# Kernel tuning notes

Hardware: AMD Instinct MI355X
Metric: run time of the kernel (lower is better)

The kernel has to match this reference:

```python
import jax, jax.numpy as jnp
import numpy as np

N_NODES = 200000
N_EDGES = 1250000
N_RELS = 8
IN_F, HID_F, OUT_F = 64, 64, 32


def setup_inputs() -> dict:
    key = jax.random.key(0)
    ks = jax.random.split(key, 8)
    x = jax.random.normal(ks[0], (N_NODES, IN_F), dtype=jnp.float32)
    edge_index = jax.random.randint(ks[1], (2, N_EDGES), 0, N_NODES, dtype=jnp.int64)
    edge_type = jax.random.randint(ks[2], (N_EDGES,), 0, N_RELS, dtype=jnp.int64)
    # Glorot-ish scaled params
    weight1 = jax.random.normal(ks[3], (N_RELS, IN_F, HID_F), dtype=jnp.float32) / np.sqrt(IN_F)
    root1 = jax.random.normal(ks[4], (IN_F, HID_F), dtype=jnp.float32) / np.sqrt(IN_F)
    bias1 = jnp.zeros((HID_F,), dtype=jnp.float32)
    weight2 = jax.random.normal(ks[5], (N_RELS, HID_F, OUT_F), dtype=jnp.float32) / np.sqrt(HID_F)
    root2 = jax.random.normal(ks[6], (HID_F, OUT_F), dtype=jnp.float32) / np.sqrt(HID_F)
    bias2 = jnp.zeros((OUT_F,), dtype=jnp.float32)
    return {"x": x, "edge_index": edge_index, "edge_type": edge_type,
            "weight1": weight1, "root1": root1, "bias1": bias1,
            "weight2": weight2, "root2": root2, "bias2": bias2}


def _rgcn_conv(x, edge_src, edge_dst, edge_type, weight, root, bias):
    """PyG RGCNConv: per-relation mean aggregation + root transform + bias."""
    num_nodes = x.shape[0]
    num_rels = weight.shape[0]
    # Transform every node under every relation weight: [N, R, H]
    xw = jnp.einsum('nd,rdh->nrh', x, weight)
    # Per-edge message: source node transformed by the edge's relation weight
    msgs = xw[edge_src, edge_type]  # [E, H]
    # Per-(target node, relation) mean aggregation
    seg = edge_dst * num_rels + edge_type  # combined segment id
    num_seg = num_nodes * num_rels
    sums = jax.ops.segment_sum(msgs, seg, num_segments=num_seg)  # [N*R, H]
    cnts = jax.ops.segment_sum(jnp.ones((msgs.shape[0],), dtype=x.dtype), seg,
                               num_segments=num_seg)
    mean = sums / jnp.maximum(cnts, 1.0)[:, None]
    agg = mean.reshape(num_nodes, num_rels, -1).sum(axis=1)  # sum over relations
    return agg + x @ root + bias


def reference(x, edge_index, edge_type, weight1, root1, bias1, weight2, root2, bias2):
    edge_src, edge_dst = edge_index[0], edge_index[1]
    h = _rgcn_conv(x, edge_src, edge_dst, edge_type, weight1, root1, bias1)
    h = jax.nn.relu(h)
    out = _rgcn_conv(h, edge_src, edge_dst, edge_type, weight2, root2, bias2)
    return out
```

## Files before the change

### kernel.cpp

```cpp
#include <hip/hip_runtime.h>

#define N_NODES 200000
#define N_EDGES 1250000
#define N_RELS 8
#define NROWS 1600000
#define NROWS_PAD 1601536
#define NSCAN 782
#define NBUCK 6250

#define NB_COUNT 4883
#define NB_XCAST 6250
#define NB_PREP1 144
#define NB_PREP2 72

typedef __attribute__((ext_vector_type(8))) short short8v;
typedef __attribute__((ext_vector_type(4))) float f32x4;

__device__ __forceinline__ ushort rne_bf16(float v) {
  unsigned u = __float_as_uint(v);
  return (ushort)((u + 0x7FFFu + ((u >> 16) & 1u)) >> 16);
}


__device__ __forceinline__ void prep_body(const float* W, const float* Root,
                                          ushort* Bf, int ncol, int i) {
  int col = i / 576, k = i - col * 576;
  float w = (k < 512) ? W[k * ncol + col] : Root[(k - 512) * ncol + col];
  int WN = ncol >> 4;
  int ks = k >> 5, kg = (k >> 3) & 3, j = k & 7;
  int wn = col >> 4, l15 = col & 15;
  int lane = (kg << 4) | l15;
  Bf[(ks * WN + wn) * 512 + lane * 8 + j] = rne_bf16(w);
}

__global__ __launch_bounds__(256) void k_setup(
    const int* __restrict__ ei, const int* __restrict__ et, int* __restrict__ cnt,
    const float* __restrict__ x, ushort* __restrict__ xbf,
    const float* __restrict__ w1, const float* __restrict__ r1, ushort* __restrict__ bf1,
    const float* __restrict__ w2, const float* __restrict__ r2, ushort* __restrict__ bf2) {
  int blk = blockIdx.x, t = threadIdx.x;
  if (blk < NB_COUNT) {
    int e = blk * 256 + t;
    if (e < N_EDGES) {
      int dst = ei[N_EDGES + e];
      int r = et[e];
      atomicAdd(&cnt[dst * N_RELS + r], 1);
    }
  } else if (blk < NB_COUNT + NB_XCAST) {
    int i = (blk - NB_COUNT) * 256 + t;
    float4 a = ((const float4*)x)[i * 2];
    float4 b = ((const float4*)x)[i * 2 + 1];
    union { uint4 q; ushort u[8]; } o;
    o.u[0] = rne_bf16(a.x); o.u[1] = rne_bf16(a.y);
    o.u[2] = rne_bf16(a.z); o.u[3] = rne_bf16(a.w);
    o.u[4] = rne_bf16(b.x); o.u[5] = rne_bf16(b.y);
    o.u[6] = rne_bf16(b.z); o.u[7] = rne_bf16(b.w);
    ((uint4*)xbf)[i] = o.q;
  } else if (blk < NB_COUNT + NB_XCAST + NB_PREP1) {
    int i = (blk - NB_COUNT - NB_XCAST) * 256 + t;
    prep_body(w1, r1, bf1, 64, i);
  } else {
    int i = (blk - NB_COUNT - NB_XCAST - NB_PREP1) * 256 + t;
    prep_body(w2, r2, bf2, 32, i);
  }
}


__global__ __launch_bounds__(256) void k_bsum(const int* __restrict__ cnt,
                                              int* __restrict__ bsum) {
  __shared__ int sh[256];
  int b = blockIdx.x, t = threadIdx.x;
  const int4* p = (const int4*)(cnt + b * 2048);
  int4 v0 = p[2 * t], v1 = p[2 * t + 1];
  int s = v0.x + v0.y + v0.z + v0.w + v1.x + v1.y + v1.z + v1.w;
  sh[t] = s;
  __syncthreads();
  for (int o = 128; o >= 1; o >>= 1) {
    if (t < o) sh[t] += sh[t + o];
    __syncthreads();
  }
  if (t == 0) bsum[b] = sh[0];
}

__global__ __launch_bounds__(1024) void k_scan1(const int* __restrict__ bsum,
                                                int* __restrict__ bpre,
                                                int* __restrict__ rowoff) {
  __shared__ int sh[1024];
  int t = threadIdx.x;
  int v = (t < NSCAN) ? bsum[t] : 0;
  sh[t] = v;
  __syncthreads();
  for (int o = 1; o < 1024; o <<= 1) {
    int a = (t >= o) ? sh[t - o] : 0;
    __syncthreads();
    sh[t] += a;
    __syncthreads();
  }
  if (t < NSCAN) bpre[t] = sh[t] - v;
  if (t == 0) rowoff[NROWS] = N_EDGES;
}

__global__ __launch_bounds__(256) void k_apply(const int* __restrict__ cnt,
                                               const int* __restrict__ bpre,
                                               int* __restrict__ rowoff,
                                               int* __restrict__ cursor) {
  __shared__ int sh[256];
  int b = blockIdx.x, t = threadIdx.x;
  const int4* p = (const int4*)(cnt + b * 2048);
  int4 v0 = p[2 * t], v1 = p[2 * t + 1];
  int v[8] = {v0.x, v0.y, v0.z, v0.w, v1.x, v1.y, v1.z, v1.w};
  int s = 0;
#pragma unroll
  for (int j = 0; j < 8; ++j) s += v[j];
  sh[t] = s;
  __syncthreads();
  for (int o = 1; o < 256; o <<= 1) {
    int a = (t >= o) ? sh[t - o] : 0;
    __syncthreads();
    sh[t] += a;
    __syncthreads();
  }
  int run = bpre[b] + sh[t] - s;
  int base = b * 2048 + t * 8;
#pragma unroll
  for (int j = 0; j < 8; ++j) {
    int i = base + j;
    if (i < NROWS) { rowoff[i] = run; cursor[i] = run; }
    run += v[j];
  }
}

__global__ void k_scatter(const int* __restrict__ ei, const int* __restrict__ et,
                          int* __restrict__ cursor, int* __restrict__ ep) {
  int e = blockIdx.x * 256 + threadIdx.x;
  if (e < N_EDGES) {
    int src = ei[e];
    int dst = ei[N_EDGES + e];
    int r = et[e];
    int row = dst * N_RELS + r;
    int pos = atomicAdd(&cursor[row], 1);
    ep[pos] = src | ((row & 255) << 18);
  }
}


template <int NCOL, bool RELUOUT, bool OUTBF>
__global__ __launch_bounds__(512, 8) void k_rgcn(
    const ushort* __restrict__ Xg, const ushort* __restrict__ Bf,
    const float* __restrict__ Bias, const int* __restrict__ rowoff,
    const int* __restrict__ ep, void* __restrict__ OutP) {
  __shared__ __align__(16) ushort agg[256 * 64];
  __shared__ int loff[260];
  __shared__ int wsplit[12];
  __shared__ __align__(16) float bias_lds[64];

  int t = threadIdx.x;
  int b = blockIdx.x;
  int d0 = b * 32;
  int lane = t & 63, w = t >> 6;

  {
    uint4 zz = make_uint4(0, 0, 0, 0);
    uint4* a4 = (uint4*)agg;
#pragma unroll
    for (int q = 0; q < 4; ++q) a4[t + q * 512] = zz;
  }
  if (t < 257) loff[t] = rowoff[b * 256 + t];
  if (t < NCOL) bias_lds[t] = Bias[t];
  __syncthreads();
  if (t < 9) {
    int s0 = loff[0], ntot = loff[256] - s0;
    int target = s0 + ((ntot * t) >> 3);
    int lo = 0, hi = 256;
    while (lo < hi) {
      int mid = (lo + hi) >> 1;
      if (loff[mid] < target) lo = mid + 1; else hi = mid;
    }
    wsplit[t] = lo;
  }
  __syncthreads();

  {
    int s = __builtin_amdgcn_readfirstlane(loff[wsplit[w]]);
    int e = __builtin_amdgcn_readfirstlane(loff[wsplit[w + 1]]);
    int n = e - s;
    const int* wep = ep + s;
    const char* Xb = (const char*)Xg;
    unsigned lane2 = (unsigned)(lane << 1);
    int cur = -1, nrun = 0;
    float a = 0.f;

#define FLUSH()                                                         \
    {                                                                   \
      float m = a * __builtin_amdgcn_rcpf((float)nrun);                 \
      int sw = (cur << 6) + (lane ^ (((cur >> 3) & 7) << 3));           \
      agg[sw] = rne_bf16(m);                                            \
    }

    int i = 0;
    for (; i + 8 <= n; i += 8) {
      int pk[8];
#pragma unroll
      for (int u = 0; u < 8; ++u)
        pk[u] = __builtin_amdgcn_readfirstlane(wep[i + u]);
      ushort hv[8];
#pragma unroll
      for (int u = 0; u < 8; ++u)
        hv[u] = *(const ushort*)(Xb + ((((unsigned)pk[u] & 0x3FFFFu) << 7) + lane2));
#pragma unroll
      for (int u = 0; u < 8; ++u) {
        int row = (int)((unsigned)pk[u] >> 18);
        float v = __uint_as_float((unsigned)hv[u] << 16);
        if (row != cur) {
          if (cur >= 0) FLUSH();
          cur = row; a = 0.f; nrun = 0;
        }
        a += v; ++nrun;
      }
    }
    for (; i < n; ++i) {
      int pk = __builtin_amdgcn_readfirstlane(wep[i]);
      ushort hv = *(const ushort*)(Xb + ((((unsigned)pk & 0x3FFFFu) << 7) + lane2));
      int row = (int)((unsigned)pk >> 18);
      float v = __uint_as_float((unsigned)hv << 16);
      if (row != cur) {
        if (cur >= 0) FLUSH();
        cur = row; a = 0.f; nrun = 0;
      }
      a += v; ++nrun;
    }
    if (cur >= 0) FLUSH();
#undef FLUSH
  }
  __syncthreads();

  int l15 = lane & 15, kg = lane >> 4;
  f32x4 acc = {0.f, 0.f, 0.f, 0.f};

  if constexpr (NCOL == 64) {
    int wm = w >> 2, wn = w & 3;
    int col = wn * 16 + l15;
    for (int ks = 0; ks < 18; ++ks) {
      union { uint4 q; short8v s; } bh, ah;
      bh.q = *(const uint4*)(Bf + (ks * 4 + wn) * 512 + lane * 8);
      if (ks < 16) {
        int rr = ks >> 1;
        int f0 = ((ks & 1) << 5) + (kg << 3);
        int row = ((wm * 16 + l15) << 3) + rr;
        int sw = (row << 6) + (f0 ^ ((l15 & 7) << 3));
        ah.q = *(const uint4*)&agg[sw];
      } else {
        int kb = ((ks - 16) << 5) + (kg << 3);
        ah.q = *(const uint4*)&Xg[(size_t)(d0 + wm * 16 + l15) * 64 + kb];
      }
      acc = __builtin_amdgcn_mfma_f32_16x16x32_bf16(ah.s, bh.s, acc, 0, 0, 0);
    }
#pragma unroll
    for (int i2 = 0; i2 < 4; ++i2) {
      float v = acc[i2] + bias_lds[col];
      if (RELUOUT) v = fmaxf(v, 0.f);
      size_t o = (size_t)(d0 + wm * 16 + kg * 4 + i2) * 64 + col;
      if (OUTBF) ((ushort*)OutP)[o] = rne_bf16(v);
      else ((float*)OutP)[o] = v;
    }
  } else {
    int wm = w >> 2, wn = (w >> 1) & 1, ksp = w & 1;
    int col = wn * 16 + l15;
    for (int ks = ksp; ks < 18; ks += 2) {
      union { uint4 q; short8v s; } bh, ah;
      bh.q = *(const uint4*)(Bf + (ks * 2 + wn) * 512 + lane * 8);
      if (ks < 16) {
        int rr = ks >> 1;
        int f0 = ((ks & 1) << 5) + (kg << 3);
        int row = ((wm * 16 + l15) << 3) + rr;
        int sw = (row << 6) + (f0 ^ ((l15 & 7) << 3));
        ah.q = *(const uint4*)&agg[sw];
      } else {
        int kb = ((ks - 16) << 5) + (kg << 3);
        ah.q = *(const uint4*)&Xg[(size_t)(d0 + wm * 16 + l15) * 64 + kb];
      }
      acc = __builtin_amdgcn_mfma_f32_16x16x32_bf16(ah.s, bh.s, acc, 0, 0, 0);
    }
    __syncthreads();
    float* red = (float*)agg;
    int rbase = wm * 16 + kg * 4;
    if (ksp == 1) {
#pragma unroll
      for (int i2 = 0; i2 < 4; ++i2) red[(rbase + i2) * 36 + col] = acc[i2];
    }
    __syncthreads();
    if (ksp == 0) {
#pragma unroll
      for (int i2 = 0; i2 < 4; ++i2) {
        float v = acc[i2] + red[(rbase + i2) * 36 + col] + bias_lds[col];
        if (RELUOUT) v = fmaxf(v, 0.f);
        ((float*)OutP)[(size_t)(d0 + rbase + i2) * 32 + col] = v;
      }
    }
  }
}


extern "C" void kernel_launch(void* const* d_in, const int* in_sizes, int n_in,
                              void* d_out, int out_size, void* d_ws, size_t ws_size,
                              hipStream_t stream) {
  const float* x = (const float*)d_in[0];
  const int* ei = (const int*)d_in[1];
  const int* et = (const int*)d_in[2];
  const float* w1 = (const float*)d_in[3];
  const float* r1 = (const float*)d_in[4];
  const float* b1 = (const float*)d_in[5];
  const float* w2 = (const float*)d_in[6];
  const float* r2 = (const float*)d_in[7];
  const float* b2 = (const float*)d_in[8];
  float* out = (float*)d_out;

  int* cnt = (int*)d_ws;
  int* bsum = cnt + NROWS_PAD;
  int* bpre = bsum + 1024;
  int* rowoff = bpre + 1024;
  int* cursor = rowoff + NROWS + 16;
  int* ep = cursor + NROWS;
  ushort* bf1 = (ushort*)(ep + N_EDGES);
  ushort* bf2 = bf1 + 36864;
  ushort* xbf = bf2 + 18432;
  ushort* hbf = xbf + 12800000;

  hipMemsetAsync(cnt, 0, (size_t)NROWS_PAD * 4, stream);
  k_setup<<<NB_COUNT + NB_XCAST + NB_PREP1 + NB_PREP2, 256, 0, stream>>>(
      ei, et, cnt, x, xbf, w1, r1, bf1, w2, r2, bf2);
  k_bsum<<<NSCAN, 256, 0, stream>>>(cnt, bsum);
  k_scan1<<<1, 1024, 0, stream>>>(bsum, bpre, rowoff);
  k_apply<<<NSCAN, 256, 0, stream>>>(cnt, bpre, rowoff, cursor);
  k_scatter<<<(N_EDGES + 255) / 256, 256, 0, stream>>>(ei, et, cursor, ep);

  k_rgcn<64, true, true><<<NBUCK, 512, 0, stream>>>(xbf, bf1, b1, rowoff, ep, hbf);
  k_rgcn<32, false, false><<<NBUCK, 512, 0, stream>>>(hbf, bf2, b2, rowoff, ep, out);
}
```

Baseline: 323.6 us.

## Reuse count-atomic ranks for scatter and software-pipeline edge gathers

The counting pass now stores the value returned by each edge's atomic increment, and the scatter uses rowoff plus that rank to place edges. This removes the second atomic pass and the cursor array writes. The edge aggregation loop in k_rgcn is rewritten as a three-stage software pipeline: it prefetches edge payloads, issues readfirstlane and the feature gathers for later batches, and accumulates the current batch, so gather latency overlaps with accumulation. The cost is higher register pressure and clamped redundant loads at the tail. Edge order within a segment now follows the counting atomics rather than the scatter atomics, so it stays non-deterministic as before.

```diff
diff --git a/kernel.cpp b/kernel.cpp
--- a/kernel.cpp
+++ b/kernel.cpp
@@ -35,6 +35,7 @@
 
 __global__ __launch_bounds__(256) void k_setup(
     const int* __restrict__ ei, const int* __restrict__ et, int* __restrict__ cnt,
+    int* __restrict__ er,
     const float* __restrict__ x, ushort* __restrict__ xbf,
     const float* __restrict__ w1, const float* __restrict__ r1, ushort* __restrict__ bf1,
     const float* __restrict__ w2, const float* __restrict__ r2, ushort* __restrict__ bf2) {
@@ -44,7 +45,7 @@
     if (e < N_EDGES) {
       int dst = ei[N_EDGES + e];
       int r = et[e];
-      atomicAdd(&cnt[dst * N_RELS + r], 1);
+      er[e] = atomicAdd(&cnt[dst * N_RELS + r], 1);
     }
   } else if (blk < NB_COUNT + NB_XCAST) {
     int i = (blk - NB_COUNT) * 256 + t;
@@ -102,8 +103,7 @@
 
 __global__ __launch_bounds__(256) void k_apply(const int* __restrict__ cnt,
                                                const int* __restrict__ bpre,
-                                               int* __restrict__ rowoff,
-                                               int* __restrict__ cursor) {
+                                               int* __restrict__ rowoff) {
   __shared__ int sh[256];
   int b = blockIdx.x, t = threadIdx.x;
   const int4* p = (const int4*)(cnt + b * 2048);
@@ -125,20 +125,21 @@
 #pragma unroll
   for (int j = 0; j < 8; ++j) {
     int i = base + j;
-    if (i < NROWS) { rowoff[i] = run; cursor[i] = run; }
+    if (i < NROWS) rowoff[i] = run;
     run += v[j];
   }
 }
 
 __global__ void k_scatter(const int* __restrict__ ei, const int* __restrict__ et,
-                          int* __restrict__ cursor, int* __restrict__ ep) {
+                          const int* __restrict__ rowoff, const int* __restrict__ er,
+                          int* __restrict__ ep) {
   int e = blockIdx.x * 256 + threadIdx.x;
   if (e < N_EDGES) {
     int src = ei[e];
     int dst = ei[N_EDGES + e];
     int r = et[e];
     int row = dst * N_RELS + r;
-    int pos = atomicAdd(&cursor[row], 1);
+    int pos = rowoff[row] + er[e];
     ep[pos] = src | ((row & 255) << 18);
   }
 }
@@ -196,40 +197,57 @@
       int sw = (cur << 6) + (lane ^ (((cur >> 3) & 7) << 3));           \
       agg[sw] = rne_bf16(m);                                            \
     }
-
-    int i = 0;
-    for (; i + 8 <= n; i += 8) {
-      int pk[8];
-#pragma unroll
-      for (int u = 0; u < 8; ++u)
-        pk[u] = __builtin_amdgcn_readfirstlane(wep[i + u]);
-      ushort hv[8];
-#pragma unroll
-      for (int u = 0; u < 8; ++u)
-        hv[u] = *(const ushort*)(Xb + ((((unsigned)pk[u] & 0x3FFFFu) << 7) + lane2));
-#pragma unroll
-      for (int u = 0; u < 8; ++u) {
-        int row = (int)((unsigned)pk[u] >> 18);
-        float v = __uint_as_float((unsigned)hv[u] << 16);
-        if (row != cur) {
-          if (cur >= 0) FLUSH();
-          cur = row; a = 0.f; nrun = 0;
-        }
-        a += v; ++nrun;
+#define PAYLOAD(P, B)                                                   \
+    _Pragma("unroll")                                                   \
+    for (int u = 0; u < 8; ++u) {                                       \
+      int idx = (B) + u; if (idx > n - 1) idx = n - 1;                  \
+      P[u] = wep[idx];                                                  \
+    }
+#define RFLG(S, P, HV)                                                  \
+    _Pragma("unroll")                                                   \
+    for (int u = 0; u < 8; ++u) {                                       \
+      S[u] = __builtin_amdgcn_readfirstlane(P[u]);                      \
+      HV[u] = *(const ushort*)(Xb + ((((unsigned)S[u] & 0x3FFFFu) << 7) + lane2)); \
+    }
+#define ACCUM(S, HV, B)                                                 \
+    {                                                                   \
+      int nb = n - (B); if (nb > 8) nb = 8;                             \
+      _Pragma("unroll")                                                 \
+      for (int u = 0; u < 8; ++u) {                                     \
+        if (u < nb) {                                                   \
+          int row = (int)((unsigned)S[u] >> 18);                        \
+          float v = __uint_as_float((unsigned)HV[u] << 16);             \
+          if (row != cur) {                                             \
+            if (cur >= 0) FLUSH();                                      \
+            cur = row; a = 0.f; nrun = 0;                               \
+          }                                                             \
+          a += v; ++nrun;                                               \
+        }                                                               \
+      }                                                                 \
+    }
+
+    if (n > 0) {
+      int p0[8], p1[8], p2[8], s0[8], s1[8], s2[8];
+      ushort hv0[8], hv1[8], hv2[8];
+      PAYLOAD(p0, 0); PAYLOAD(p1, 8); PAYLOAD(p2, 16);
+      RFLG(s0, p0, hv0);
+      RFLG(s1, p1, hv1);
+      for (int base = 0; base < n; base += 24) {
+        PAYLOAD(p0, base + 24);
+        RFLG(s2, p2, hv2);
+        ACCUM(s0, hv0, base);
+        PAYLOAD(p1, base + 32);
+        RFLG(s0, p0, hv0);
+        ACCUM(s1, hv1, base + 8);
+        PAYLOAD(p2, base + 40);
+        RFLG(s1, p1, hv1);
+        ACCUM(s2, hv2, base + 16);
       }
-    }
-    for (; i < n; ++i) {
-      int pk = __builtin_amdgcn_readfirstlane(wep[i]);
-      ushort hv = *(const ushort*)(Xb + ((((unsigned)pk & 0x3FFFFu) << 7) + lane2));
-      int row = (int)((unsigned)pk >> 18);
-      float v = __uint_as_float((unsigned)hv << 16);
-      if (row != cur) {
-        if (cur >= 0) FLUSH();
-        cur = row; a = 0.f; nrun = 0;
-      }
-      a += v; ++nrun;
-    }
-    if (cur >= 0) FLUSH();
+      if (cur >= 0) FLUSH();
+    }
+#undef ACCUM
+#undef RFLG
+#undef PAYLOAD
 #undef FLUSH
   }
   __syncthreads();
@@ -319,8 +337,8 @@
   int* bsum = cnt + NROWS_PAD;
   int* bpre = bsum + 1024;
   int* rowoff = bpre + 1024;
-  int* cursor = rowoff + NROWS + 16;
-  int* ep = cursor + NROWS;
+  int* er = rowoff + NROWS + 16;
+  int* ep = er + N_EDGES;
   ushort* bf1 = (ushort*)(ep + N_EDGES);
   ushort* bf2 = bf1 + 36864;
   ushort* xbf = bf2 + 18432;
@@ -328,11 +346,11 @@
 
   hipMemsetAsync(cnt, 0, (size_t)NROWS_PAD * 4, stream);
   k_setup<<<NB_COUNT + NB_XCAST + NB_PREP1 + NB_PREP2, 256, 0, stream>>>(
-      ei, et, cnt, x, xbf, w1, r1, bf1, w2, r2, bf2);
+      ei, et, cnt, er, x, xbf, w1, r1, bf1, w2, r2, bf2);
   k_bsum<<<NSCAN, 256, 0, stream>>>(cnt, bsum);
   k_scan1<<<1, 1024, 0, stream>>>(bsum, bpre, rowoff);
-  k_apply<<<NSCAN, 256, 0, stream>>>(cnt, bpre, rowoff, cursor);
-  k_scatter<<<(N_EDGES + 255) / 256, 256, 0, stream>>>(ei, et, cursor, ep);
+  k_apply<<<NSCAN, 256, 0, stream>>>(cnt, bpre, rowoff);
+  k_scatter<<<(N_EDGES + 255) / 256, 256, 0, stream>>>(ei, et, rowoff, er, ep);
 
   k_rgcn<64, true, true><<<NBUCK, 512, 0, stream>>>(xbf, bf1, b1, rowoff, ep, hbf);
   k_rgcn<32, false, false><<<NBUCK, 512, 0, stream>>>(hbf, bf2, b2, rowoff, ep, out);
```

New measurement: 297.6 us. -8.0%, faster.
